# Performance work log

Measured on AMD Instinct MI355X. Metric: run time of the kernel, lower is better.

The kernel has to match this reference:

```python
import jax, jax.numpy as jnp
import numpy as np

NEG = -1e9  # matches deepblast's -1e10-style boundary fill, fp32-safe


def nw_terminal(theta, A):
    # Soft Needleman-Wunsch forward pass with the softmax (logsumexp) operator,
    # vectorized as an anti-diagonal wavefront scan.
    # theta, A: [N, M]. Returns terminal value V[N, M].
    # Recursion (deepblast): V[i,j] = theta[i-1,j-1] +
    #   lse(A[i-1,j-1] + V[i-1,j], V[i-1,j-1], A[i-1,j-1] + V[i,j-1])
    N, M = theta.shape
    ii = jnp.arange(N + 1)  # row index along a diagonal
    prev2 = jnp.full((N + 1,), NEG, theta.dtype).at[0].set(0.0)  # diagonal k=0: V[0,0]=0
    prev1 = jnp.full((N + 1,), NEG, theta.dtype)                  # diagonal k=1: boundary
    neg1 = jnp.full((1,), NEG, theta.dtype)

    def step(carry, k):
        p2, p1 = carry
        jj = k - ii
        valid = (ii >= 1) & (jj >= 1) & (jj <= M)
        ti = jnp.clip(ii - 1, 0, N - 1)
        tj = jnp.clip(jj - 1, 0, M - 1)
        th = theta[ti, tj]
        a = A[ti, tj]
        up = jnp.concatenate([neg1, p1[:-1]])    # V[i-1, j]
        left = p1                                 # V[i, j-1]
        diag = jnp.concatenate([neg1, p2[:-1]])   # V[i-1, j-1]
        v = jax.nn.logsumexp(jnp.stack([a + up, diag, a + left]), axis=0)
        cur = jnp.where(valid, th + v, NEG)
        return (p1, cur), None

    (_, last), _ = jax.lax.scan(step, (prev2, prev1), jnp.arange(2, N + M + 1))
    return last[N]  # V[N, M]


def nw_decode(theta, A):
    # Expected alignment matrix = d V_terminal / d theta, exactly what
    # NWDecoderCUDA.decode computes via its forward/backward DP passes
    # (gradient taken w.r.t. theta only; A is held fixed).
    f = lambda th: jnp.sum(jax.vmap(nw_terminal)(th, A))
    return jax.grad(f)(theta)


def setup_inputs() -> dict:
    key = jax.random.key(0)
    k1, k2, k3, k4 = jax.random.split(key, 4)
    B, N, M, D = 8, 512, 512, 512
    s = 1.0 / np.sqrt(D)  # keep bilinear scores O(1), as trained embeddings would be
    return {
        "zx": jax.random.normal(k1, (B, N, D), jnp.float32) * s,
        "zy": jax.random.normal(k2, (B, M, D), jnp.float32) * s,
        "gx": jax.random.normal(k3, (B, N, D), jnp.float32) * s,
        "gy": jax.random.normal(k4, (B, M, D), jnp.float32) * s,
    }


def reference(zx, zy, gx, gy):
    theta = jax.nn.softplus(jnp.einsum('bid,bjd->bij', zx, zy))  # match scores [B,N,M]
    A = jax.nn.log_sigmoid(jnp.einsum('bid,bjd->bij', gx, gy))   # gap scores   [B,N,M]
    aln = nw_decode(theta, A)                                     # soft alignment [B,N,M]
    return aln, theta, A
```

## Files before the change

### kernel.cpp

```cpp
#include <hip/hip_runtime.h>
#include <cmath>

#define NEG -1e9f
#define LOG2E 1.44269504088896340736f
constexpr int B = 8, N = 512, M = 512, D = 512;
constexpr size_t NM = (size_t)N * M;

constexpr int NCHUNK = 72;

#define EXP2F(x) __builtin_amdgcn_exp2f(x)
#define LOG2F(x) __builtin_amdgcn_logf(x)

typedef float f32x2 __attribute__((ext_vector_type(2)));

__device__ __forceinline__ float dpp_shr1(float v) {
    return __int_as_float(__builtin_amdgcn_update_dpp(
        __float_as_int(v), __float_as_int(v), 0x138, 0xf, 0xf, false));
}
__device__ __forceinline__ float dpp_shl1(float v) {
    return __int_as_float(__builtin_amdgcn_update_dpp(
        __float_as_int(v), __float_as_int(v), 0x130, 0xf, 0xf, false));
}

__device__ __forceinline__ int diag_off(int kd) {
    return (kd <= 511) ? ((kd * (kd + 1)) >> 1)
                       : ((int)NM - (((1023 - kd) * (1024 - kd)) >> 1));
}

__global__ __launch_bounds__(256)
void gemm_act_kernel(const float* __restrict__ zx, const float* __restrict__ zy,
                     const float* __restrict__ gx, const float* __restrict__ gy,
                     float* __restrict__ out_theta, float* __restrict__ out_A)
{
    const int bz = blockIdx.z;
    const int b = bz >> 1, which = bz & 1;
    const float* X = (which ? gx : zx) + (size_t)b * N * D;
    const float* Y = (which ? gy : zy) + (size_t)b * M * D;
    float* C = (which ? out_A : out_theta) + (size_t)b * NM;

    __shared__ float Xs[16][68];
    __shared__ float Ys[16][68];

    const int tx = threadIdx.x, ty = threadIdx.y;
    const int t = ty * 16 + tx;
    const int lrow = t >> 2;
    const int lk4 = (t & 3) * 4;
    const int row0 = blockIdx.y * 64, col0 = blockIdx.x * 64;

    float acc[4][4] = {};

    for (int k0 = 0; k0 < D; k0 += 16) {
        const float4 xv = *(const float4*)&X[(row0 + lrow) * D + k0 + lk4];
        const float4 yv = *(const float4*)&Y[(col0 + lrow) * D + k0 + lk4];
        Xs[lk4 + 0][lrow] = xv.x; Xs[lk4 + 1][lrow] = xv.y;
        Xs[lk4 + 2][lrow] = xv.z; Xs[lk4 + 3][lrow] = xv.w;
        Ys[lk4 + 0][lrow] = yv.x; Ys[lk4 + 1][lrow] = yv.y;
        Ys[lk4 + 2][lrow] = yv.z; Ys[lk4 + 3][lrow] = yv.w;
        __syncthreads();
#pragma unroll
        for (int kk = 0; kk < 16; kk++) {
            const float4 a = *(const float4*)&Xs[kk][ty * 4];
            const float4 bb = *(const float4*)&Ys[kk][tx * 4];
            acc[0][0] += a.x * bb.x; acc[0][1] += a.x * bb.y; acc[0][2] += a.x * bb.z; acc[0][3] += a.x * bb.w;
            acc[1][0] += a.y * bb.x; acc[1][1] += a.y * bb.y; acc[1][2] += a.y * bb.z; acc[1][3] += a.y * bb.w;
            acc[2][0] += a.z * bb.x; acc[2][1] += a.z * bb.y; acc[2][2] += a.z * bb.z; acc[2][3] += a.z * bb.w;
            acc[3][0] += a.w * bb.x; acc[3][1] += a.w * bb.y; acc[3][2] += a.w * bb.z; acc[3][3] += a.w * bb.w;
        }
        __syncthreads();
    }

#pragma unroll
    for (int r = 0; r < 4; r++) {
        float4 o;
        float* op = &o.x;
#pragma unroll
        for (int c = 0; c < 4; c++) {
            const float x = acc[r][c];
            const float l = log1pf(expf(-fabsf(x)));
            op[c] = which ? (fminf(x, 0.0f) - l)
                          : (fmaxf(x, 0.0f) + l);
        }
        *(float4*)&C[(size_t)(row0 + ty * 4 + r) * M + col0 + tx * 4] = o;
    }
}

__global__ __launch_bounds__(256)
void reorder_in_kernel(const float* __restrict__ theta, const float* __restrict__ A,
                       float2* __restrict__ TAD)
{
    __shared__ float T[64][67];
    __shared__ float Ag[64][67];
    const int b = blockIdx.z;
    const float* ts = theta + (size_t)b * NM;
    const float* as = A + (size_t)b * NM;
    float2* dst = TAD + (size_t)b * NM;
    const int r0 = blockIdx.y * 64, c0 = blockIdx.x * 64;
    const int t = threadIdx.x, lane = t & 63, wv = t >> 6;

#pragma unroll
    for (int e = 0; e < 16; e++) {
        const int r = wv * 16 + e;
        T[r][lane]  = ts[(size_t)(r0 + r) * M + c0 + lane];
        Ag[r][lane] = as[(size_t)(r0 + r) * M + c0 + lane];
    }
    __syncthreads();
    for (int dd = wv; dd < 127; dd += 4) {
        const int kd = r0 + c0 + dd;
        const int rlo = max(0, dd - 63);
        const int L = min(63, dd) - rlo + 1;
        if (lane < L) {
            const int rloc = rlo + lane;
            const int gr = r0 + rloc;
            dst[diag_off(kd) + gr - max(0, kd - 511)] =
                make_float2(T[rloc][dd - rloc] * LOG2E, Ag[rloc][dd - rloc] * LOG2E);
        }
    }
}

__global__ __launch_bounds__(256)
void reorder_out_kernel(const float* __restrict__ ED, float* __restrict__ aln)
{
    __shared__ float T[64][67];
    const int b = blockIdx.z;
    const float* src = ED + (size_t)b * NM;
    float* dst = aln + (size_t)b * NM;
    const int r0 = blockIdx.y * 64, c0 = blockIdx.x * 64;
    const int t = threadIdx.x, lane = t & 63, wv = t >> 6;

    for (int dd = wv; dd < 127; dd += 4) {
        const int kd = r0 + c0 + dd;
        const int rlo = max(0, dd - 63);
        const int L = min(63, dd) - rlo + 1;
        if (lane < L) {
            const int rloc = rlo + lane;
            const int gr = r0 + rloc;
            T[rloc][dd - rloc] = src[diag_off(kd) + gr - max(0, kd - 511)];
        }
    }
    __syncthreads();
#pragma unroll
    for (int e = 0; e < 16; e++) {
        const int r = wv * 16 + e;
        dst[(size_t)(r0 + r) * M + c0 + lane] = T[r][lane];
    }
}

#define VMCNT_TOP                              \
    asm volatile("s_waitcnt vmcnt(0)");        \
    __builtin_amdgcn_sched_barrier(0);

#define CHUNK_BARRIER                          \
    __builtin_amdgcn_sched_barrier(0);         \
    asm volatile("s_waitcnt lgkmcnt(0)");      \
    __builtin_amdgcn_s_barrier();              \
    __builtin_amdgcn_sched_barrier(0);

#define DECL16(P)  f32x2 P##0, P##1, P##2, P##3, P##4, P##5, P##6, P##7, \
                         P##8, P##9, P##10, P##11, P##12, P##13, P##14, P##15;
#define DECL16F(P) float P##0, P##1, P##2, P##3, P##4, P##5, P##6, P##7, \
                         P##8, P##9, P##10, P##11, P##12, P##13, P##14, P##15;

#define FLOAD1(dst) {                                          \
    asm volatile("global_load_dwordx2 %0, %1, %2"              \
                 : "=v"(dst) : "v"(off8l), "s"(tab));          \
    const int d_ = (kdl <= 510) ? max(kdl + 1, 0)              \
                                : max(1022 - kdl, 0);          \
    off8l += d_ * 8; kdl++;                                    \
}
#define F_ISSUE(P) {                                           \
    FLOAD1(P##0)  FLOAD1(P##1)  FLOAD1(P##2)  FLOAD1(P##3)     \
    FLOAD1(P##4)  FLOAD1(P##5)  FLOAD1(P##6)  FLOAD1(P##7)     \
    FLOAD1(P##8)  FLOAD1(P##9)  FLOAD1(P##10) FLOAD1(P##11)    \
    FLOAD1(P##12) FLOAD1(P##13) FLOAD1(P##14) FLOAD1(P##15)    \
}

#define F_CORE(kd_, TA, sh1v, dgv, O) {                        \
    const float th = (TA).x, a = (TA).y;                       \
    const float x0 = a + sh1v;                                 \
    const float x2 = a + vprev;                                \
    const float mx = fmaxf(fmaxf(x0, dgv), x2);                \
    const float e0 = EXP2F(x0 - mx);                           \
    const float e1 = EXP2F(dgv - mx);                          \
    const float e2 = EXP2F(x2 - mx);                           \
    const float sum = e0 + e1 + e2;                            \
    const float inv = __builtin_amdgcn_rcpf(sum);              \
    (O).x = e0 * inv; (O).y = e2 * inv;                        \
    vprev = th + mx + LOG2F(sum);                              \
    if (lane == 63) ring[w][(kd_) & 63] = vprev;               \
}

#define F_STEP_I(s, TA, O, RG) {                               \
    const int kd = kb + (s);                                   \
    float sh1 = dpp_shr1(vprev);                               \
    if (lane == 0) sh1 = RG;                                   \
    const float dgv = sh1_d;                                   \
    sh1_d = sh1;                                               \
    F_CORE(kd, TA, sh1, dgv, O)                                \
}

#define F_STEP_G(s, TA, O, RG) {                               \
    const int kd = kb + (s);                                   \
    const int jj = kd - tid;                                   \
    float sh1 = dpp_shr1(vprev);                               \
    if (lane == 0) sh1 = RG;                                   \
    const float dgv = (jj == 0) ? ((tid == 0) ? 0.0f : NEG) : sh1_d; \
    sh1_d = sh1;                                               \
    if (jj >= 0 && jj < M) { F_CORE(kd, TA, sh1, dgv, O) }     \
}

#define F_STEPS(SFX, CUR)                                                    \
    F_STEP_##SFX(0,  CUR##0,  o0,  r0)  F_STEP_##SFX(1,  CUR##1,  o1,  r1)   \
    F_STEP_##SFX(2,  CUR##2,  o2,  r2)  F_STEP_##SFX(3,  CUR##3,  o3,  r3)   \
    F_STEP_##SFX(4,  CUR##4,  o4,  r4)  F_STEP_##SFX(5,  CUR##5,  o5,  r5)   \
    F_STEP_##SFX(6,  CUR##6,  o6,  r6)  F_STEP_##SFX(7,  CUR##7,  o7,  r7)   \
    F_STEP_##SFX(8,  CUR##8,  o8,  r8)  F_STEP_##SFX(9,  CUR##9,  o9,  r9)   \
    F_STEP_##SFX(10, CUR##10, o10, r10) F_STEP_##SFX(11, CUR##11, o11, r11)  \
    F_STEP_##SFX(12, CUR##12, o12, r12) F_STEP_##SFX(13, CUR##13, o13, r13)  \
    F_STEP_##SFX(14, CUR##14, o14, r14) F_STEP_##SFX(15, CUR##15, o15, r15)

#define F_ADV_S { const int d_ = (kds <= 510) ? (kds + 1) : (1022 - kds);    \
                  off8s += d_ * 8; kds++; }
#define FST_I(O) {                                                           \
    asm volatile("global_store_dwordx2 %0, %1, %2"                           \
                 :: "v"(off8s), "v"(O), "s"(pb) : "memory");                 \
    F_ADV_S }
#define FST_G(s, O) {                                                        \
    const int jj = kb + (s) - tid;                                           \
    if (jj >= 0 && jj < M) {                                                 \
        asm volatile("global_store_dwordx2 %0, %1, %2"                       \
                     :: "v"(off8s), "v"(O), "s"(pb) : "memory"); }           \
    F_ADV_S }
#define F_STORES_I {                                                         \
    FST_I(o0)  FST_I(o1)  FST_I(o2)  FST_I(o3)                               \
    FST_I(o4)  FST_I(o5)  FST_I(o6)  FST_I(o7)                               \
    FST_I(o8)  FST_I(o9)  FST_I(o10) FST_I(o11)                              \
    FST_I(o12) FST_I(o13) FST_I(o14) FST_I(o15) }
#define F_STORES_G {                                                         \
    FST_G(0,o0)   FST_G(1,o1)   FST_G(2,o2)   FST_G(3,o3)                    \
    FST_G(4,o4)   FST_G(5,o5)   FST_G(6,o6)   FST_G(7,o7)                    \
    FST_G(8,o8)   FST_G(9,o9)   FST_G(10,o10) FST_G(11,o11)                  \
    FST_G(12,o12) FST_G(13,o13) FST_G(14,o14) FST_G(15,o15) }

#define F_CHUNK(c_, CUR, NXT) {                                \
    const int c = (c_);                                        \
    VMCNT_TOP                         \
    F_ISSUE(NXT)               \
    if (c >= ca && c <= cb) {                                  \
        const int kb = 16 * c - w16;                           \
        float r0 = NEG, r1 = NEG, r2 = NEG, r3 = NEG,          \
              r4 = NEG, r5 = NEG, r6 = NEG, r7 = NEG,          \
              r8 = NEG, r9 = NEG, r10 = NEG, r11 = NEG,        \
              r12 = NEG, r13 = NEG, r14 = NEG, r15 = NEG;      \
        if (w > 0) {                                           \
            r0  = ring[w - 1][(kb - 1) & 63];                  \
            r1  = ring[w - 1][(kb + 0) & 63];                  \
            r2  = ring[w - 1][(kb + 1) & 63];                  \
            r3  = ring[w - 1][(kb + 2) & 63];                  \
            r4  = ring[w - 1][(kb + 3) & 63];                  \
            r5  = ring[w - 1][(kb + 4) & 63];                  \
            r6  = ring[w - 1][(kb + 5) & 63];                  \
            r7  = ring[w - 1][(kb + 6) & 63];                  \
            r8  = ring[w - 1][(kb + 7) & 63];                  \
            r9  = ring[w - 1][(kb + 8) & 63];                  \
            r10 = ring[w - 1][(kb + 9) & 63];                  \
            r11 = ring[w - 1][(kb + 10) & 63];                 \
            r12 = ring[w - 1][(kb + 11) & 63];                 \
            r13 = ring[w - 1][(kb + 12) & 63];                 \
            r14 = ring[w - 1][(kb + 13) & 63];                 \
            r15 = ring[w - 1][(kb + 14) & 63];                 \
        }                                                      \
        DECL16(o)                                              \
        const int kr = kb - 64 * w;                            \
        if (kr >= 64 && kr <= 496) {                           \
            F_STEPS(I, CUR)                                    \
            F_STORES_I                                         \
        } else {                                               \
            F_STEPS(G, CUR)                                    \
            F_STORES_G                                         \
        }                                                      \
    }                                                          \
    CHUNK_BARRIER                                              \
}

__global__ __launch_bounds__(512, 1)
void nw_forward_kernel(const float2* __restrict__ TAD, float2* __restrict__ pD)
{
    __shared__ float ring[8][64];
    const int b = blockIdx.x;
    const int tid = threadIdx.x;
    const int w = __builtin_amdgcn_readfirstlane(tid >> 6);
    const int lane = tid & 63;
    const int w16 = 16 * w;
    const float2* tab = TAD + (size_t)b * NM;
    float2* pb = pD + (size_t)b * NM;

    for (int x = tid; x < 8 * 64; x += 512) ((float*)ring)[x] = NEG;
    __syncthreads();

    const int ca = 5 * w, cb = 5 * w + 35;

    int kdl = -w16;
    int off8l = tid * 8;
    int kds = 64 * w;
    int off8s = (((kds * (kds + 1)) >> 1) + tid) * 8;

    DECL16(fa) DECL16(fb)
    F_ISSUE(fa)

    float vprev = NEG, sh1_d = NEG;

#pragma unroll 1
    for (int c2 = 0; c2 < NCHUNK; c2 += 2) {
        F_CHUNK(c2 + 0, fa, fb)
        F_CHUNK(c2 + 1, fb, fa)
    }
}

#define BLOAD1(dst) {                                          \
    asm volatile("global_load_dwordx2 %0, %1, %2"              \
                 : "=v"(dst) : "v"(off8l), "s"(pbp));          \
    const int d_ = (kdl <= 511) ? (-max(kdl, 0))               \
                                : min(kdl - 1023, 0);          \
    off8l += d_ * 8; kdl--;                                    \
}
#define B_ISSUE(P) {                                           \
    BLOAD1(P##0)  BLOAD1(P##1)  BLOAD1(P##2)  BLOAD1(P##3)     \
    BLOAD1(P##4)  BLOAD1(P##5)  BLOAD1(P##6)  BLOAD1(P##7)     \
    BLOAD1(P##8)  BLOAD1(P##9)  BLOAD1(P##10) BLOAD1(P##11)    \
    BLOAD1(P##12) BLOAD1(P##13) BLOAD1(P##14) BLOAD1(P##15)    \
}

#define B_CORE(kd_, PP, suv, sdv, EV, TERMFIX) {               \
    float e = suv + sdv + ql1;                                 \
    TERMFIX                                                    \
    const float pu = (PP).x, pl = (PP).y;                      \
    const float pd = 1.0f - pu - pl;                           \
    const float qu = pu * e, qd = pd * e, ql = pl * e;         \
    EV = e;                                                    \
    qd2 = qd1; qd1 = qd; qu1 = qu; ql1 = ql;                   \
    if (lane == 0) {                                           \
        ring_u[w][(kd_) & 63] = qu;                            \
        ring_d[w][(kd_) & 63] = qd;                            \
    }                                                          \
}

#define B_STEP_I(s, PP, EV, RU, RD) {                          \
    const int kd = kb - (s);                                   \
    float su = dpp_shl1(qu1);                                  \
    float sd = dpp_shl1(qd2);                                  \
    if (lane == 63) { su = RU; sd = RD; }                      \
    B_CORE(kd, PP, su, sd, EV, )                               \
}

#define B_STEP_G(s, PP, EV, RU, RD) {                          \
    const int kd = kb - (s);                                   \
    const int jj = kd - tid;                                   \
    float su = dpp_shl1(qu1);                                  \
    float sd = dpp_shl1(qd2);                                  \
    if (lane == 63) { su = RU; sd = RD; }                      \
    if (jj >= 0 && jj < M) {                                   \
        B_CORE(kd, PP, su, sd, EV,                             \
               if (tid == N - 1 && jj == M - 1) e = 1.0f;)     \
    }                                                          \
}

#define B_STEPS(SFX, CUR)                                                          \
    B_STEP_##SFX(0,  CUR##0,  ev0,  ru0,  rd0)  B_STEP_##SFX(1,  CUR##1,  ev1,  ru1,  rd1)  \
    B_STEP_##SFX(2,  CUR##2,  ev2,  ru2,  rd2)  B_STEP_##SFX(3,  CUR##3,  ev3,  ru3,  rd3)  \
    B_STEP_##SFX(4,  CUR##4,  ev4,  ru4,  rd4)  B_STEP_##SFX(5,  CUR##5,  ev5,  ru5,  rd5)  \
    B_STEP_##SFX(6,  CUR##6,  ev6,  ru6,  rd6)  B_STEP_##SFX(7,  CUR##7,  ev7,  ru7,  rd7)  \
    B_STEP_##SFX(8,  CUR##8,  ev8,  ru8,  rd8)  B_STEP_##SFX(9,  CUR##9,  ev9,  ru9,  rd9)  \
    B_STEP_##SFX(10, CUR##10, ev10, ru10, rd10) B_STEP_##SFX(11, CUR##11, ev11, ru11, rd11) \
    B_STEP_##SFX(12, CUR##12, ev12, ru12, rd12) B_STEP_##SFX(13, CUR##13, ev13, ru13, rd13) \
    B_STEP_##SFX(14, CUR##14, ev14, ru14, rd14) B_STEP_##SFX(15, CUR##15, ev15, ru15, rd15)

#define B_ADV_S { const int d_ = (kds <= 511) ? (-max(kds, 0))               \
                                              : min(kds - 1023, 0);          \
                  off4s += d_ * 4; kds--; }
#define BST_I(EV) {                                                          \
    asm volatile("global_store_dword %0, %1, %2"                             \
                 :: "v"(off4s), "v"(EV), "s"(ebp) : "memory");               \
    B_ADV_S }
#define BST_G(s, EV) {                                                       \
    const int jj = kb - (s) - tid;                                           \
    if (jj >= 0 && jj < M) {                                                 \
        asm volatile("global_store_dword %0, %1, %2"                         \
                     :: "v"(off4s), "v"(EV), "s"(ebp) : "memory"); }         \
    B_ADV_S }
#define B_STORES_I {                                                         \
    BST_I(ev0)  BST_I(ev1)  BST_I(ev2)  BST_I(ev3)                           \
    BST_I(ev4)  BST_I(ev5)  BST_I(ev6)  BST_I(ev7)                           \
    BST_I(ev8)  BST_I(ev9)  BST_I(ev10) BST_I(ev11)                          \
    BST_I(ev12) BST_I(ev13) BST_I(ev14) BST_I(ev15) }
#define B_STORES_G {                                                         \
    BST_G(0,ev0)   BST_G(1,ev1)   BST_G(2,ev2)   BST_G(3,ev3)                \
    BST_G(4,ev4)   BST_G(5,ev5)   BST_G(6,ev6)   BST_G(7,ev7)                \
    BST_G(8,ev8)   BST_G(9,ev9)   BST_G(10,ev10) BST_G(11,ev11)              \
    BST_G(12,ev12) BST_G(13,ev13) BST_G(14,ev14) BST_G(15,ev15) }

#define B_CHUNK(c_, CUR, NXT) {                                \
    const int c = (c_);                                        \
    VMCNT_TOP                                                  \
    B_ISSUE(NXT)                                               \
    if (c >= ca && c <= cb) {                                  \
        const int kb = 1134 - 16 * c - w16;                    \
        float ru0 = 0.f, ru1 = 0.f, ru2 = 0.f, ru3 = 0.f,      \
              ru4 = 0.f, ru5 = 0.f, ru6 = 0.f, ru7 = 0.f,      \
              ru8 = 0.f, ru9 = 0.f, ru10 = 0.f, ru11 = 0.f,    \
              ru12 = 0.f, ru13 = 0.f, ru14 = 0.f, ru15 = 0.f;  \
        float rd0 = 0.f, rd1 = 0.f, rd2 = 0.f, rd3 = 0.f,      \
              rd4 = 0.f, rd5 = 0.f, rd6 = 0.f, rd7 = 0.f,      \
              rd8 = 0.f, rd9 = 0.f, rd10 = 0.f, rd11 = 0.f,    \
              rd12 = 0.f, rd13 = 0.f, rd14 = 0.f, rd15 = 0.f;  \
        if (w < 7) {                                           \
            ru0  = ring_u[w + 1][(kb + 1)  & 63]; rd0  = ring_d[w + 1][(kb + 2)  & 63]; \
            ru1  = ring_u[w + 1][(kb + 0)  & 63]; rd1  = ring_d[w + 1][(kb + 1)  & 63]; \
            ru2  = ring_u[w + 1][(kb - 1)  & 63]; rd2  = ring_d[w + 1][(kb + 0)  & 63]; \
            ru3  = ring_u[w + 1][(kb - 2)  & 63]; rd3  = ring_d[w + 1][(kb - 1)  & 63]; \
            ru4  = ring_u[w + 1][(kb - 3)  & 63]; rd4  = ring_d[w + 1][(kb - 2)  & 63]; \
            ru5  = ring_u[w + 1][(kb - 4)  & 63]; rd5  = ring_d[w + 1][(kb - 3)  & 63]; \
            ru6  = ring_u[w + 1][(kb - 5)  & 63]; rd6  = ring_d[w + 1][(kb - 4)  & 63]; \
            ru7  = ring_u[w + 1][(kb - 6)  & 63]; rd7  = ring_d[w + 1][(kb - 5)  & 63]; \
            ru8  = ring_u[w + 1][(kb - 7)  & 63]; rd8  = ring_d[w + 1][(kb - 6)  & 63]; \
            ru9  = ring_u[w + 1][(kb - 8)  & 63]; rd9  = ring_d[w + 1][(kb - 7)  & 63]; \
            ru10 = ring_u[w + 1][(kb - 9)  & 63]; rd10 = ring_d[w + 1][(kb - 8)  & 63]; \
            ru11 = ring_u[w + 1][(kb - 10) & 63]; rd11 = ring_d[w + 1][(kb - 9)  & 63]; \
            ru12 = ring_u[w + 1][(kb - 11) & 63]; rd12 = ring_d[w + 1][(kb - 10) & 63]; \
            ru13 = ring_u[w + 1][(kb - 12) & 63]; rd13 = ring_d[w + 1][(kb - 11) & 63]; \
            ru14 = ring_u[w + 1][(kb - 13) & 63]; rd14 = ring_d[w + 1][(kb - 12) & 63]; \
            ru15 = ring_u[w + 1][(kb - 14) & 63]; rd15 = ring_d[w + 1][(kb - 13) & 63]; \
        }                                                      \
        DECL16F(ev)                                            \
        const int krb = kb - 64 * w;                           \
        if (krb >= 78 && krb <= 511) {                         \
            B_STEPS(I, CUR)                                    \
            B_STORES_I                                         \
        } else {                                               \
            B_STEPS(G, CUR)                                    \
            B_STORES_G                                         \
        }                                                      \
    }                                                          \
    CHUNK_BARRIER                                              \
}

__global__ __launch_bounds__(512, 1)
void nw_backward_kernel(const float2* __restrict__ pD, float* __restrict__ ED)
{
    __shared__ float ring_u[8][64];
    __shared__ float ring_d[8][64];
    const int b = blockIdx.x;
    const int tid = threadIdx.x;
    const int w = __builtin_amdgcn_readfirstlane(tid >> 6);
    const int lane = tid & 63;
    const int w16 = 16 * w;
    const float2* pbp = pD + (size_t)b * NM;
    float* ebp = ED + (size_t)b * NM;

    for (int x = tid; x < 8 * 64; x += 512) {
        ((float*)ring_u)[x] = 0.0f;
        ((float*)ring_d)[x] = 0.0f;
    }
    __syncthreads();

    const int ca = 35 - 5 * w, cb = 70 - 5 * w;

    int kdl = 1134 - w16;
    int off8l = ((int)NM - 512 + tid) * 8;
    int kds = 574 + 64 * w;
    const int am_ = 1023 - kds, bm_ = 1024 - kds;
    int off4s = ((int)NM - ((am_ * bm_) >> 1) + tid - (kds - 511)) * 4;

    DECL16(ba) DECL16(bb)
    B_ISSUE(ba)

    float qu1 = 0.0f, qd1 = 0.0f, qd2 = 0.0f, ql1 = 0.0f;

#pragma unroll 1
    for (int c2 = 0; c2 < NCHUNK; c2 += 2) {
        B_CHUNK(c2 + 0, ba, bb)
        B_CHUNK(c2 + 1, bb, ba)
    }
}

extern "C" void kernel_launch(void* const* d_in, const int* in_sizes, int n_in,
                              void* d_out, int out_size, void* d_ws, size_t ws_size,
                              hipStream_t stream) {
    const float* zx = (const float*)d_in[0];
    const float* zy = (const float*)d_in[1];
    const float* gx = (const float*)d_in[2];
    const float* gy = (const float*)d_in[3];

    float* aln   = (float*)d_out;
    float* theta = aln + B * NM;
    float* Amat  = theta + B * NM;

    float2* TAD = (float2*)d_ws;
    float2* pD  = TAD + B * NM;
    float*  ED  = (float*)d_ws;

    gemm_act_kernel<<<dim3(8, 8, B * 2), dim3(16, 16), 0, stream>>>(zx, zy, gx, gy, theta, Amat);
    reorder_in_kernel<<<dim3(8, 8, B), 256, 0, stream>>>(theta, Amat, TAD);
    nw_forward_kernel<<<B, 512, 0, stream>>>(TAD, pD);
    nw_backward_kernel<<<B, 512, 0, stream>>>(pD, ED);
    reorder_out_kernel<<<dim3(8, 8, B), 256, 0, stream>>>(ED, aln);
}
```

Baseline: 558.0 us.

## Batch inter-wave ring exchange into float4 LDS ops and relax vmcnt waits

The forward and backward wavefront kernels no longer write a boundary value to the LDS ring on every step. Each chunk's 16 boundary values are buffered in registers and written once as four float4 stores. The neighbour's values are read as float4 vectors, with a carried element to cover the one-step offset. The chunk-top wait is relaxed to vmcnt(16) after interior chunks, so the next chunk's prefetch stays in flight. This cuts per-step LDS traffic and wait stalls, at the cost of more live registers and more complex carry bookkeeping.

```diff
diff --git a/kernel.cpp b/kernel.cpp
--- a/kernel.cpp
+++ b/kernel.cpp
@@ -12,6 +12,9 @@
 #define LOG2F(x) __builtin_amdgcn_logf(x)
 
 typedef float f32x2 __attribute__((ext_vector_type(2)));
+
+#define GLOAD(dst, ptr) \
+    asm volatile("global_load_dwordx2 %0, %1, off" : "=v"(dst) : "v"(ptr))
 
 __device__ __forceinline__ float dpp_shr1(float v) {
     return __int_as_float(__builtin_amdgcn_update_dpp(
@@ -145,8 +148,9 @@
     }
 }
 
-#define VMCNT_TOP                              \
-    asm volatile("s_waitcnt vmcnt(0)");        \
+#define VMCNT_TOP_PF                                        \
+    if (pf) { asm volatile("s_waitcnt vmcnt(16)"); }        \
+    else    { asm volatile("s_waitcnt vmcnt(0)");  }        \
     __builtin_amdgcn_sched_barrier(0);
 
 #define CHUNK_BARRIER                          \
@@ -186,16 +190,15 @@
     const float inv = __builtin_amdgcn_rcpf(sum);              \
     (O).x = e0 * inv; (O).y = e2 * inv;                        \
     vprev = th + mx + LOG2F(sum);                              \
-    if (lane == 63) ring[w][(kd_) & 63] = vprev;               \
 }
 
 #define F_STEP_I(s, TA, O, RG) {                               \
-    const int kd = kb + (s);                                   \
     float sh1 = dpp_shr1(vprev);                               \
     if (lane == 0) sh1 = RG;                                   \
     const float dgv = sh1_d;                                   \
     sh1_d = sh1;                                               \
-    F_CORE(kd, TA, sh1, dgv, O)                                \
+    F_CORE(kb + (s), TA, sh1, dgv, O)                          \
+    wv##s = vprev;                                             \
 }
 
 #define F_STEP_G(s, TA, O, RG) {                               \
@@ -206,17 +209,18 @@
     const float dgv = (jj == 0) ? ((tid == 0) ? 0.0f : NEG) : sh1_d; \
     sh1_d = sh1;                                               \
     if (jj >= 0 && jj < M) { F_CORE(kd, TA, sh1, dgv, O) }     \
-}
-
-#define F_STEPS(SFX, CUR)                                                    \
-    F_STEP_##SFX(0,  CUR##0,  o0,  r0)  F_STEP_##SFX(1,  CUR##1,  o1,  r1)   \
-    F_STEP_##SFX(2,  CUR##2,  o2,  r2)  F_STEP_##SFX(3,  CUR##3,  o3,  r3)   \
-    F_STEP_##SFX(4,  CUR##4,  o4,  r4)  F_STEP_##SFX(5,  CUR##5,  o5,  r5)   \
-    F_STEP_##SFX(6,  CUR##6,  o6,  r6)  F_STEP_##SFX(7,  CUR##7,  o7,  r7)   \
-    F_STEP_##SFX(8,  CUR##8,  o8,  r8)  F_STEP_##SFX(9,  CUR##9,  o9,  r9)   \
-    F_STEP_##SFX(10, CUR##10, o10, r10) F_STEP_##SFX(11, CUR##11, o11, r11)  \
-    F_STEP_##SFX(12, CUR##12, o12, r12) F_STEP_##SFX(13, CUR##13, o13, r13)  \
-    F_STEP_##SFX(14, CUR##14, o14, r14) F_STEP_##SFX(15, CUR##15, o15, r15)
+    wv##s = vprev;                                             \
+}
+
+#define F_STEPS(SFX, CUR)                                                      \
+    F_STEP_##SFX(0,  CUR##0,  o0,  rgP) F_STEP_##SFX(1,  CUR##1,  o1,  g0)     \
+    F_STEP_##SFX(2,  CUR##2,  o2,  g1)  F_STEP_##SFX(3,  CUR##3,  o3,  g2)     \
+    F_STEP_##SFX(4,  CUR##4,  o4,  g3)  F_STEP_##SFX(5,  CUR##5,  o5,  g4)     \
+    F_STEP_##SFX(6,  CUR##6,  o6,  g5)  F_STEP_##SFX(7,  CUR##7,  o7,  g6)     \
+    F_STEP_##SFX(8,  CUR##8,  o8,  g7)  F_STEP_##SFX(9,  CUR##9,  o9,  g8)     \
+    F_STEP_##SFX(10, CUR##10, o10, g9)  F_STEP_##SFX(11, CUR##11, o11, g10)    \
+    F_STEP_##SFX(12, CUR##12, o12, g11) F_STEP_##SFX(13, CUR##13, o13, g12)    \
+    F_STEP_##SFX(14, CUR##14, o14, g13) F_STEP_##SFX(15, CUR##15, o15, g14)
 
 #define F_ADV_S { const int d_ = (kds <= 510) ? (kds + 1) : (1022 - kds);    \
                   off8s += d_ * 8; kds++; }
@@ -243,49 +247,49 @@
 
 #define F_CHUNK(c_, CUR, NXT) {                                \
     const int c = (c_);                                        \
-    VMCNT_TOP                         \
+    VMCNT_TOP_PF                      \
     F_ISSUE(NXT)               \
-    if (c >= ca && c <= cb) {                                  \
-        const int kb = 16 * c - w16;                           \
-        float r0 = NEG, r1 = NEG, r2 = NEG, r3 = NEG,          \
-              r4 = NEG, r5 = NEG, r6 = NEG, r7 = NEG,          \
-              r8 = NEG, r9 = NEG, r10 = NEG, r11 = NEG,        \
-              r12 = NEG, r13 = NEG, r14 = NEG, r15 = NEG;      \
-        if (w > 0) {                                           \
-            r0  = ring[w - 1][(kb - 1) & 63];                  \
-            r1  = ring[w - 1][(kb + 0) & 63];                  \
-            r2  = ring[w - 1][(kb + 1) & 63];                  \
-            r3  = ring[w - 1][(kb + 2) & 63];                  \
-            r4  = ring[w - 1][(kb + 3) & 63];                  \
-            r5  = ring[w - 1][(kb + 4) & 63];                  \
-            r6  = ring[w - 1][(kb + 5) & 63];                  \
-            r7  = ring[w - 1][(kb + 6) & 63];                  \
-            r8  = ring[w - 1][(kb + 7) & 63];                  \
-            r9  = ring[w - 1][(kb + 8) & 63];                  \
-            r10 = ring[w - 1][(kb + 9) & 63];                  \
-            r11 = ring[w - 1][(kb + 10) & 63];                 \
-            r12 = ring[w - 1][(kb + 11) & 63];                 \
-            r13 = ring[w - 1][(kb + 12) & 63];                 \
-            r14 = ring[w - 1][(kb + 13) & 63];                 \
-            r15 = ring[w - 1][(kb + 14) & 63];                 \
-        }                                                      \
+    const int kb = 16 * c - w16;                               \
+    const int kr = kb - 64 * w;                                \
+    const bool act = (c >= ca && c <= cb);                     \
+    const bool interior = act && (kr >= 64) && (kr <= 496);    \
+    const float rgP = gcar;                                    \
+    if (w > 0 && c >= ca - 1 && c <= cb) {                     \
+        const float4* rp = (const float4*)&ring[w - 1][kb & 63]; \
+        const float4 A0 = rp[0], A1 = rp[1];                   \
+        const float4 A2 = rp[2], A3 = rp[3];                   \
+        g0  = A0.x; g1  = A0.y; g2  = A0.z; g3  = A0.w;        \
+        g4  = A1.x; g5  = A1.y; g6  = A1.z; g7  = A1.w;        \
+        g8  = A2.x; g9  = A2.y; g10 = A2.z; g11 = A2.w;        \
+        g12 = A3.x; g13 = A3.y; g14 = A3.z; g15 = A3.w;        \
+        gcar = g15;                                            \
+    }                                                          \
+    if (act) {                                                 \
+        DECL16F(wv)                                            \
         DECL16(o)                                              \
-        const int kr = kb - 64 * w;                            \
-        if (kr >= 64 && kr <= 496) {                           \
+        if (interior) {                                        \
             F_STEPS(I, CUR)                                    \
             F_STORES_I                                         \
         } else {                                               \
             F_STEPS(G, CUR)                                    \
             F_STORES_G                                         \
         }                                                      \
+        if (lane == 63) {                                      \
+            float4* wp = (float4*)&ring[w][kb & 63];           \
+            wp[0] = make_float4(wv0,  wv1,  wv2,  wv3);        \
+            wp[1] = make_float4(wv4,  wv5,  wv6,  wv7);        \
+            wp[2] = make_float4(wv8,  wv9,  wv10, wv11);       \
+            wp[3] = make_float4(wv12, wv13, wv14, wv15);       \
+        }                                                      \
     }                                                          \
+    pf = interior;                                             \
     CHUNK_BARRIER                                              \
 }
 
 __global__ __launch_bounds__(512, 1)
 void nw_forward_kernel(const float2* __restrict__ TAD, float2* __restrict__ pD)
 {
-    __shared__ float ring[8][64];
+    __shared__ __align__(16) float ring[8][64];
     const int b = blockIdx.x;
     const int tid = threadIdx.x;
     const int w = __builtin_amdgcn_readfirstlane(tid >> 6);
@@ -307,7 +311,12 @@
     DECL16(fa) DECL16(fb)
     F_ISSUE(fa)
 
+    float g0 = NEG, g1 = NEG, g2 = NEG, g3 = NEG, g4 = NEG, g5 = NEG,
+          g6 = NEG, g7 = NEG, g8 = NEG, g9 = NEG, g10 = NEG, g11 = NEG,
+          g12 = NEG, g13 = NEG, g14 = NEG, g15 = NEG, gcar = NEG;
+
     float vprev = NEG, sh1_d = NEG;
+    bool pf = false;
 
 #pragma unroll 1
     for (int c2 = 0; c2 < NCHUNK; c2 += 2) {
@@ -338,18 +347,14 @@
     const float qu = pu * e, qd = pd * e, ql = pl * e;         \
     EV = e;                                                    \
     qd2 = qd1; qd1 = qd; qu1 = qu; ql1 = ql;                   \
-    if (lane == 0) {                                           \
-        ring_u[w][(kd_) & 63] = qu;                            \
-        ring_d[w][(kd_) & 63] = qd;                            \
-    }                                                          \
 }
 
 #define B_STEP_I(s, PP, EV, RU, RD) {                          \
-    const int kd = kb - (s);                                   \
     float su = dpp_shl1(qu1);                                  \
     float sd = dpp_shl1(qd2);                                  \
     if (lane == 63) { su = RU; sd = RD; }                      \
-    B_CORE(kd, PP, su, sd, EV, )                               \
+    B_CORE(kb - (s), PP, su, sd, EV, )                         \
+    wu##s = qu1; wd##s = qd1;                                  \
 }
 
 #define B_STEP_G(s, PP, EV, RU, RD) {                          \
@@ -362,17 +367,26 @@
         B_CORE(kd, PP, su, sd, EV,                             \
                if (tid == N - 1 && jj == M - 1) e = 1.0f;)     \
     }                                                          \
-}
-
-#define B_STEPS(SFX, CUR)                                                          \
-    B_STEP_##SFX(0,  CUR##0,  ev0,  ru0,  rd0)  B_STEP_##SFX(1,  CUR##1,  ev1,  ru1,  rd1)  \
-    B_STEP_##SFX(2,  CUR##2,  ev2,  ru2,  rd2)  B_STEP_##SFX(3,  CUR##3,  ev3,  ru3,  rd3)  \
-    B_STEP_##SFX(4,  CUR##4,  ev4,  ru4,  rd4)  B_STEP_##SFX(5,  CUR##5,  ev5,  ru5,  rd5)  \
-    B_STEP_##SFX(6,  CUR##6,  ev6,  ru6,  rd6)  B_STEP_##SFX(7,  CUR##7,  ev7,  ru7,  rd7)  \
-    B_STEP_##SFX(8,  CUR##8,  ev8,  ru8,  rd8)  B_STEP_##SFX(9,  CUR##9,  ev9,  ru9,  rd9)  \
-    B_STEP_##SFX(10, CUR##10, ev10, ru10, rd10) B_STEP_##SFX(11, CUR##11, ev11, ru11, rd11) \
-    B_STEP_##SFX(12, CUR##12, ev12, ru12, rd12) B_STEP_##SFX(13, CUR##13, ev13, ru13, rd13) \
-    B_STEP_##SFX(14, CUR##14, ev14, ru14, rd14) B_STEP_##SFX(15, CUR##15, ev15, ru15, rd15)
+    wu##s = qu1; wd##s = qd1;                                  \
+}
+
+#define B_STEPS(SFX, CUR)                                        \
+    B_STEP_##SFX(0,  CUR##0,  ev0,  cuP,  cAP)                   \
+    B_STEP_##SFX(1,  CUR##1,  ev1,  gu15, cBP)                   \
+    B_STEP_##SFX(2,  CUR##2,  ev2,  gu14, gd15)                  \
+    B_STEP_##SFX(3,  CUR##3,  ev3,  gu13, gd14)                  \
+    B_STEP_##SFX(4,  CUR##4,  ev4,  gu12, gd13)                  \
+    B_STEP_##SFX(5,  CUR##5,  ev5,  gu11, gd12)                  \
+    B_STEP_##SFX(6,  CUR##6,  ev6,  gu10, gd11)                  \
+    B_STEP_##SFX(7,  CUR##7,  ev7,  gu9,  gd10)                  \
+    B_STEP_##SFX(8,  CUR##8,  ev8,  gu8,  gd9)                   \
+    B_STEP_##SFX(9,  CUR##9,  ev9,  gu7,  gd8)                   \
+    B_STEP_##SFX(10, CUR##10, ev10, gu6,  gd7)                   \
+    B_STEP_##SFX(11, CUR##11, ev11, gu5,  gd6)                   \
+    B_STEP_##SFX(12, CUR##12, ev12, gu4,  gd5)                   \
+    B_STEP_##SFX(13, CUR##13, ev13, gu3,  gd4)                   \
+    B_STEP_##SFX(14, CUR##14, ev14, gu2,  gd3)                   \
+    B_STEP_##SFX(15, CUR##15, ev15, gu1,  gd2)
 
 #define B_ADV_S { const int d_ = (kds <= 511) ? (-max(kds, 0))               \
                                               : min(kds - 1023, 0);          \
@@ -400,54 +414,63 @@
 
 #define B_CHUNK(c_, CUR, NXT) {                                \
     const int c = (c_);                                        \
-    VMCNT_TOP                                                  \
+    VMCNT_TOP_PF                                               \
     B_ISSUE(NXT)                                               \
-    if (c >= ca && c <= cb) {                                  \
-        const int kb = 1134 - 16 * c - w16;                    \
-        float ru0 = 0.f, ru1 = 0.f, ru2 = 0.f, ru3 = 0.f,      \
-              ru4 = 0.f, ru5 = 0.f, ru6 = 0.f, ru7 = 0.f,      \
-              ru8 = 0.f, ru9 = 0.f, ru10 = 0.f, ru11 = 0.f,    \
-              ru12 = 0.f, ru13 = 0.f, ru14 = 0.f, ru15 = 0.f;  \
-        float rd0 = 0.f, rd1 = 0.f, rd2 = 0.f, rd3 = 0.f,      \
-              rd4 = 0.f, rd5 = 0.f, rd6 = 0.f, rd7 = 0.f,      \
-              rd8 = 0.f, rd9 = 0.f, rd10 = 0.f, rd11 = 0.f,    \
-              rd12 = 0.f, rd13 = 0.f, rd14 = 0.f, rd15 = 0.f;  \
-        if (w < 7) {                                           \
-            ru0  = ring_u[w + 1][(kb + 1)  & 63]; rd0  = ring_d[w + 1][(kb + 2)  & 63]; \
-            ru1  = ring_u[w + 1][(kb + 0)  & 63]; rd1  = ring_d[w + 1][(kb + 1)  & 63]; \
-            ru2  = ring_u[w + 1][(kb - 1)  & 63]; rd2  = ring_d[w + 1][(kb + 0)  & 63]; \
-            ru3  = ring_u[w + 1][(kb - 2)  & 63]; rd3  = ring_d[w + 1][(kb - 1)  & 63]; \
-            ru4  = ring_u[w + 1][(kb - 3)  & 63]; rd4  = ring_d[w + 1][(kb - 2)  & 63]; \
-            ru5  = ring_u[w + 1][(kb - 4)  & 63]; rd5  = ring_d[w + 1][(kb - 3)  & 63]; \
-            ru6  = ring_u[w + 1][(kb - 5)  & 63]; rd6  = ring_d[w + 1][(kb - 4)  & 63]; \
-            ru7  = ring_u[w + 1][(kb - 6)  & 63]; rd7  = ring_d[w + 1][(kb - 5)  & 63]; \
-            ru8  = ring_u[w + 1][(kb - 7)  & 63]; rd8  = ring_d[w + 1][(kb - 6)  & 63]; \
-            ru9  = ring_u[w + 1][(kb - 8)  & 63]; rd9  = ring_d[w + 1][(kb - 7)  & 63]; \
-            ru10 = ring_u[w + 1][(kb - 9)  & 63]; rd10 = ring_d[w + 1][(kb - 8)  & 63]; \
-            ru11 = ring_u[w + 1][(kb - 10) & 63]; rd11 = ring_d[w + 1][(kb - 9)  & 63]; \
-            ru12 = ring_u[w + 1][(kb - 11) & 63]; rd12 = ring_d[w + 1][(kb - 10) & 63]; \
-            ru13 = ring_u[w + 1][(kb - 12) & 63]; rd13 = ring_d[w + 1][(kb - 11) & 63]; \
-            ru14 = ring_u[w + 1][(kb - 13) & 63]; rd14 = ring_d[w + 1][(kb - 12) & 63]; \
-            ru15 = ring_u[w + 1][(kb - 14) & 63]; rd15 = ring_d[w + 1][(kb - 13) & 63]; \
-        }                                                      \
-        DECL16F(ev)                                            \
-        const int krb = kb - 64 * w;                           \
-        if (krb >= 78 && krb <= 511) {                         \
+    const int kb = 1134 - 16 * c - w16;                        \
+    const int krb = kb - 64 * w;                               \
+    const bool act = (c >= ca && c <= cb);                     \
+    const bool interior = act && (krb >= 78) && (krb <= 511);  \
+    const float cuP = cu, cAP = cA, cBP = cB;                  \
+    if (w < 7 && c >= ca - 1 && c <= cb) {                     \
+        const int rb = (kb - 14) & 63;                         \
+        const float4* up = (const float4*)&ring_u[w + 1][rb];  \
+        const float4 U0 = up[0], U1 = up[1];                   \
+        const float4 U2 = up[2], U3 = up[3];                   \
+        gu0  = U0.x; gu1  = U0.y; gu2  = U0.z; gu3  = U0.w;    \
+        gu4  = U1.x; gu5  = U1.y; gu6  = U1.z; gu7  = U1.w;    \
+        gu8  = U2.x; gu9  = U2.y; gu10 = U2.z; gu11 = U2.w;    \
+        gu12 = U3.x; gu13 = U3.y; gu14 = U3.z; gu15 = U3.w;    \
+        const float4* dp = (const float4*)&ring_d[w + 1][rb];  \
+        const float4 D0 = dp[0], D1 = dp[1];                   \
+        const float4 D2 = dp[2], D3 = dp[3];                   \
+        gd0  = D0.x; gd1  = D0.y; gd2  = D0.z; gd3  = D0.w;    \
+        gd4  = D1.x; gd5  = D1.y; gd6  = D1.z; gd7  = D1.w;    \
+        gd8  = D2.x; gd9  = D2.y; gd10 = D2.z; gd11 = D2.w;    \
+        gd12 = D3.x; gd13 = D3.y; gd14 = D3.z; gd15 = D3.w;    \
+        cu = gu0; cA = gd1; cB = gd0;                          \
+    }                                                          \
+    if (act) {                                                 \
+        DECL16F(wu) DECL16F(wd) DECL16F(ev)                    \
+        if (interior) {                                        \
             B_STEPS(I, CUR)                                    \
             B_STORES_I                                         \
         } else {                                               \
             B_STEPS(G, CUR)                                    \
             B_STORES_G                                         \
         }                                                      \
+        if (lane == 0) {                                       \
+            const int rb2 = (kb - 14) & 63;                    \
+            float4* au = (float4*)&ring_u[w][rb2];             \
+            au[0] = make_float4(wu15, wu14, wu13, wu12);       \
+            au[1] = make_float4(wu11, wu10, wu9,  wu8);        \
+            au[2] = make_float4(wu7,  wu6,  wu5,  wu4);        \
+            au[3] = make_float4(wu3,  wu2,  wu1,  wu0);        \
+            float4* ad = (float4*)&ring_d[w][rb2];             \
+            ad[0] = make_float4(wd15, wd14, wd13, wd12);       \
+            ad[1] = make_float4(wd11, wd10, wd9,  wd8);        \
+            ad[2] = make_float4(wd7,  wd6,  wd5,  wd4);        \
+            ad[3] = make_float4(wd3,  wd2,  wd1,  wd0);        \
+        }                                                      \
     }                                                          \
+    pf = interior;                                             \
     CHUNK_BARRIER                                              \
 }
 
 __global__ __launch_bounds__(512, 1)
 void nw_backward_kernel(const float2* __restrict__ pD, float* __restrict__ ED)
 {
-    __shared__ float ring_u[8][64];
-    __shared__ float ring_d[8][64];
+    __shared__ __align__(16) float ring_u[8][64];
+    __shared__ __align__(16) float ring_d[8][64];
     const int b = blockIdx.x;
     const int tid = threadIdx.x;
     const int w = __builtin_amdgcn_readfirstlane(tid >> 6);
@@ -473,7 +496,16 @@
     DECL16(ba) DECL16(bb)
     B_ISSUE(ba)
 
+    float gu0 = 0.f, gu1 = 0.f, gu2 = 0.f, gu3 = 0.f, gu4 = 0.f, gu5 = 0.f,
+          gu6 = 0.f, gu7 = 0.f, gu8 = 0.f, gu9 = 0.f, gu10 = 0.f, gu11 = 0.f,
+          gu12 = 0.f, gu13 = 0.f, gu14 = 0.f, gu15 = 0.f;
+    float gd0 = 0.f, gd1 = 0.f, gd2 = 0.f, gd3 = 0.f, gd4 = 0.f, gd5 = 0.f,
+          gd6 = 0.f, gd7 = 0.f, gd8 = 0.f, gd9 = 0.f, gd10 = 0.f, gd11 = 0.f,
+          gd12 = 0.f, gd13 = 0.f, gd14 = 0.f, gd15 = 0.f;
+    float cu = 0.f, cA = 0.f, cB = 0.f;
+
     float qu1 = 0.0f, qd1 = 0.0f, qd2 = 0.0f, ql1 = 0.0f;
+    bool pf = false;
 
 #pragma unroll 1
     for (int c2 = 0; c2 < NCHUNK; c2 += 2) {
```

Result: faster. 502.8 us (-9.9%).
